# Optimization experiments

Measured on AMD Instinct MI355X. Metric: run time of the kernel, lower is better.

Reference implementation:

```python
import jax, jax.numpy as jnp
import numpy as np

NL, D, H, DFF = 6, 1024, 16, 4096
HD = D // H


def _rope(x):
    # x: [B, L, H, HD]; rotate-half RoPE applied along seq dim 1
    L = x.shape[1]
    half = HD // 2
    inv = 1.0 / (10000.0 ** (jnp.arange(half, dtype=jnp.float32) / half))
    ang = jnp.arange(L, dtype=jnp.float32)[:, None] * inv  # [L, half]
    cos = jnp.cos(ang)[None, :, None, :]
    sin = jnp.sin(ang)[None, :, None, :]
    x1, x2 = x[..., :half], x[..., half:]
    return jnp.concatenate([x1 * cos - x2 * sin, x1 * sin + x2 * cos], axis=-1)


def _ln(x, eps=1e-5):
    m = jnp.mean(x, axis=-1, keepdims=True)
    v = jnp.var(x, axis=-1, keepdims=True)
    return (x - m) * jax.lax.rsqrt(v + eps)


def _adaln(x, emb, w, b):
    # emb: [B,1,D] -> squeeze; proj -> gamma,beta
    gb = emb[:, 0, :] @ w.T + b  # [B, 2D]
    g, be = jnp.split(gb, 2, axis=-1)
    return _ln(x) * (1.0 + g[:, None, :]) + be[:, None, :]


def _attn(q, k, v, mask):
    # q:[B,Lq,H,HD] k,v:[B,Lkv,H,HD] mask:[B,Lkv] True=ignore
    scores = jnp.einsum('bqhd,bkhd->bhqk', q, k) / np.float32(np.sqrt(HD))
    scores = jnp.where(mask[:, None, None, :], jnp.float32(-jnp.inf), scores)
    w = jax.nn.softmax(scores, axis=-1)
    return jnp.einsum('bhqk,bkhd->bqhd', w, v)


def setup_inputs() -> dict:
    key = jax.random.key(0)
    ks = jax.random.split(key, 20)
    B, L, LC = 4, 1024, 512
    s = 0.02
    inp = {
        'x': jax.random.normal(ks[0], (B, L, D), jnp.float32),
        'noise_emb': jax.random.normal(ks[1], (B, 1, D), jnp.float32),
        'context': jax.random.normal(ks[2], (B, LC, D), jnp.float32),
        'src_mask': jnp.zeros((B, L), bool),
        'ctx_mask': jnp.zeros((B, LC), bool),
        'n1_w': jax.random.normal(ks[3], (NL, 2 * D, D), jnp.float32) * s,
        'n1_b': jnp.zeros((NL, 2 * D), jnp.float32),
        'n2_w': jax.random.normal(ks[4], (NL, 2 * D, D), jnp.float32) * s,
        'n2_b': jnp.zeros((NL, 2 * D), jnp.float32),
        'n3_w': jax.random.normal(ks[5], (NL, 2 * D, D), jnp.float32) * s,
        'n3_b': jnp.zeros((NL, 2 * D), jnp.float32),
        'qkv_w': jax.random.normal(ks[6], (NL, 3 * D, D), jnp.float32) * s,
        'so_w': jax.random.normal(ks[7], (NL, D, D), jnp.float32) * s,
        'cq_w': jax.random.normal(ks[8], (NL, D, D), jnp.float32) * s,
        'ck_w': jax.random.normal(ks[9], (NL, D, D), jnp.float32) * s,
        'cv_w': jax.random.normal(ks[10], (NL, D, D), jnp.float32) * s,
        'co_w': jax.random.normal(ks[11], (NL, D, D), jnp.float32) * s,
        'f1_w': jax.random.normal(ks[12], (NL, DFF, D), jnp.float32) * s,
        'f1_b': jnp.zeros((NL, DFF), jnp.float32),
        'f2_w': jax.random.normal(ks[13], (NL, D, DFF), jnp.float32) * s,
        'f2_b': jnp.zeros((NL, D), jnp.float32),
    }
    return inp


def reference(x, noise_emb, context, src_mask, ctx_mask,
              n1_w, n1_b, n2_w, n2_b, n3_w, n3_b,
              qkv_w, so_w, cq_w, ck_w, cv_w, co_w,
              f1_w, f1_b, f2_w, f2_b):
    B, L, _ = x.shape
    LC = context.shape[1]
    for i in range(NL):
        # self-attention with AdaLN pre-norm
        xn = _adaln(x, noise_emb, n1_w[i], n1_b[i])
        qkv = xn @ qkv_w[i].T  # [B,L,3D]
        q, k, v = jnp.split(qkv, 3, axis=-1)
        q = _rope(q.reshape(B, L, H, HD))
        k = _rope(k.reshape(B, L, H, HD))
        v = v.reshape(B, L, H, HD)
        a = _attn(q, k, v, src_mask).reshape(B, L, D) @ so_w[i].T
        x = x + a
        # cross-attention with AdaLN pre-norm
        xn = _adaln(x, noise_emb, n2_w[i], n2_b[i])
        q = _rope((xn @ cq_w[i].T).reshape(B, L, H, HD))
        k = _rope((context @ ck_w[i].T).reshape(B, LC, H, HD))
        v = (context @ cv_w[i].T).reshape(B, LC, H, HD)
        a = _attn(q, k, v, ctx_mask).reshape(B, L, D) @ co_w[i].T
        x = x + a
        # FFN with AdaLN pre-norm
        xn = _adaln(x, noise_emb, n3_w[i], n3_b[i])
        h = jax.nn.gelu(xn @ f1_w[i].T + f1_b[i], approximate=False)
        x = x + (h @ f2_w[i].T + f2_b[i])
    return x
```

## Files before the change

### kernel.cpp

```cpp
#include <hip/hip_runtime.h>
#include <hip/hip_bf16.h>
#include <math.h>

#define D_    1024
#define H_    16
#define HD_   64
#define NL_   6
#define DFF_  4096
#define B_    4
#define L_    1024
#define LC_   512

typedef short bf16x8 __attribute__((ext_vector_type(8)));
typedef float f32x4  __attribute__((ext_vector_type(4)));
typedef unsigned int uint32;

__device__ __forceinline__ float waveReduceSum(float v) {
#pragma unroll
  for (int off = 32; off > 0; off >>= 1) v += __shfl_xor(v, off);
  return v;
}
__device__ __forceinline__ ushort f2bf(float f) {
  union { __hip_bfloat16 h; ushort u; } c;
  c.h = __float2bfloat16(f);
  return c.u;
}
__device__ __forceinline__ float bf2f(ushort u) {
  union { uint32 i; float f; } c;
  c.i = ((uint32)u) << 16;
  return c.f;
}
__device__ __forceinline__ uint32 pk2(float a, float b) {
  return (uint32)f2bf(a) | ((uint32)f2bf(b) << 16);
}
__device__ __forceinline__ void gload16(const ushort* g, ushort* l) {
  __builtin_amdgcn_global_load_lds(
      (const __attribute__((address_space(1))) uint32*)g,
      (__attribute__((address_space(3))) uint32*)l, 16, 0, 0);
}

__global__ __launch_bounds__(256) void cvt_bf16_kernel(
    const float* __restrict__ in, ushort* __restrict__ out, int n4) {
  int i = blockIdx.x * 256 + threadIdx.x;
  int stride = gridDim.x * 256;
  for (; i < n4; i += stride) {
    float4 v = ((const float4*)in)[i];
    ushort4 o = {f2bf(v.x), f2bf(v.y), f2bf(v.z), f2bf(v.w)};
    ((ushort4*)out)[i] = o;
  }
}

__global__ __launch_bounds__(256) void cvt_pack_kv_kernel(
    const float* __restrict__ ck, const float* __restrict__ cv,
    ushort* __restrict__ out, int n4) {
  int i = blockIdx.x * 256 + threadIdx.x;
  int stride = gridDim.x * 256;
  for (; i < n4; i += stride) {
    int row = i >> 8;
    int cb = i & 255;
    int layer = row >> 11;
    int sel = (row >> 10) & 1;
    int r = row & 1023;
    const float* src = (sel ? cv : ck) +
                       (((size_t)layer << 10) + r) * 1024 + cb * 4;
    float4 v = *(const float4*)src;
    ushort4 o = {f2bf(v.x), f2bf(v.y), f2bf(v.z), f2bf(v.w)};
    ((ushort4*)out)[i] = o;
  }
}

__global__ void rope_table_kernel(float* __restrict__ tab) {
  int t = blockIdx.x * 256 + threadIdx.x;
  if (t >= L_ * 32) return;
  int l = t >> 5, j = t & 31;
  float inv = powf(10000.f, -(float)j * (1.f / 32.f));
  float ang = (float)l * inv;
  tab[l * 64 + j] = cosf(ang);
  tab[l * 64 + 32 + j] = sinf(ang);
}

__global__ __launch_bounds__(256) void adaln_gb_all_kernel(
    const float* __restrict__ emb,
    const float* __restrict__ n1w, const float* __restrict__ n2w,
    const float* __restrict__ n3w,
    const float* __restrict__ n1b, const float* __restrict__ n2b,
    const float* __restrict__ n3b,
    float* __restrict__ gb) {
  int wid = blockIdx.x * 4 + (threadIdx.x >> 6);
  int lane = threadIdx.x & 63;
  int n = wid & 2047;
  int g = wid >> 11;
  int layer = g / 3, j = g - layer * 3;
  const float* wbase = (j == 0 ? n1w : (j == 1 ? n2w : n3w));
  const float* bbase = (j == 0 ? n1b : (j == 1 ? n2b : n3b));
  const float* wr = wbase + ((size_t)layer * 2048 + n) * 1024;
  float s0 = 0.f, s1 = 0.f, s2 = 0.f, s3 = 0.f;
#pragma unroll
  for (int k4 = 0; k4 < 4; ++k4) {
    int idx = k4 * 64 + lane;
    float4 w4 = ((const float4*)wr)[idx];
    float4 e0 = ((const float4*)emb)[idx];
    float4 e1 = ((const float4*)(emb + 1024))[idx];
    float4 e2 = ((const float4*)(emb + 2048))[idx];
    float4 e3 = ((const float4*)(emb + 3072))[idx];
    s0 += w4.x * e0.x + w4.y * e0.y + w4.z * e0.z + w4.w * e0.w;
    s1 += w4.x * e1.x + w4.y * e1.y + w4.z * e1.z + w4.w * e1.w;
    s2 += w4.x * e2.x + w4.y * e2.y + w4.z * e2.z + w4.w * e2.w;
    s3 += w4.x * e3.x + w4.y * e3.y + w4.z * e3.z + w4.w * e3.w;
  }
  s0 = waveReduceSum(s0);
  s1 = waveReduceSum(s1);
  s2 = waveReduceSum(s2);
  s3 = waveReduceSum(s3);
  if (lane == 0) {
    float bb = bbase[(size_t)layer * 2048 + n];
    gb[((size_t)g * 4 + 0) * 2048 + n] = s0 + bb;
    gb[((size_t)g * 4 + 1) * 2048 + n] = s1 + bb;
    gb[((size_t)g * 4 + 2) * 2048 + n] = s2 + bb;
    gb[((size_t)g * 4 + 3) * 2048 + n] = s3 + bb;
  }
}

__global__ __launch_bounds__(256) void adaln_apply_kernel(
    const float* __restrict__ x, const float* __restrict__ gb,
    ushort* __restrict__ xn) {
  int r = blockIdx.x;
  int b = r >> 10;
  const float* xr = x + (size_t)r * D_;
  int tid = threadIdx.x;
  float4 v = *(const float4*)(xr + tid * 4);
  float s = v.x + v.y + v.z + v.w;
  float q = v.x * v.x + v.y * v.y + v.z * v.z + v.w * v.w;
  s = waveReduceSum(s);
  q = waveReduceSum(q);
  __shared__ float ssum[4], ssq[4], stats[2];
  int w = tid >> 6, lane = tid & 63;
  if (lane == 0) { ssum[w] = s; ssq[w] = q; }
  __syncthreads();
  if (tid == 0) {
    float S = ssum[0] + ssum[1] + ssum[2] + ssum[3];
    float Q = ssq[0] + ssq[1] + ssq[2] + ssq[3];
    float mean = S * (1.f / D_);
    float var = Q * (1.f / D_) - mean * mean;
    stats[0] = mean;
    stats[1] = rsqrtf(var + 1e-5f);
  }
  __syncthreads();
  float mean = stats[0], rstd = stats[1];
  const float* gp = gb + (size_t)b * 2048;
  float4 g  = *(const float4*)(gp + tid * 4);
  float4 be = *(const float4*)(gp + D_ + tid * 4);
  ushort4 o;
  o.x = f2bf((v.x - mean) * rstd * (1.f + g.x) + be.x);
  o.y = f2bf((v.y - mean) * rstd * (1.f + g.y) + be.y);
  o.z = f2bf((v.z - mean) * rstd * (1.f + g.z) + be.z);
  o.w = f2bf((v.w - mean) * rstd * (1.f + g.w) + be.w);
  *(ushort4*)(xn + (size_t)r * D_ + tid * 4) = o;
}

template <int FLAGS, bool OUTBF, int ROPE>
__global__ __launch_bounds__(256) void gemm_mfma_kernel(
    const ushort* __restrict__ A, int lda,
    const ushort* __restrict__ W, int ldw,
    const float* __restrict__ bias,
    const float* __restrict__ res, int ldres,
    void* __restrict__ Cout, int ldc, int K,
    const float* __restrict__ tab, int rlim, int lmask) {
  __shared__ __align__(16) ushort lds[24576];
  const int tid = threadIdx.x;
  const int lane = tid & 63, wv = tid >> 6;
  const int wrow = (wv >> 1) * 64, wcol = (wv & 1) * 64;
  const int fr = lane & 15;
  const int kbs = (((lane >> 4) ^ (fr & 3)) & 3) * 8;

  const int nwg = gridDim.x * gridDim.y;
  const int wg = blockIdx.y * gridDim.x + blockIdx.x;
  const int q = nwg >> 3;
  const int swz = (wg & 7) * q + (wg >> 3);
  const int row0 = (swz / gridDim.x) * 128;
  const int col0 = (swz % gridDim.x) * 128;

  const int c0 = wv * 2, c1 = wv * 2 + 1;
  const int sr = lane >> 2;
  const int sc = (((lane & 3) ^ (sr & 3)) & 3) * 8;
  const ushort* Ap0 = A + (size_t)(row0 + c0 * 16 + sr) * lda + sc;
  const ushort* Ap1 = A + (size_t)(row0 + c1 * 16 + sr) * lda + sc;
  const ushort* Wp0 = W + (size_t)(col0 + c0 * 16 + sr) * ldw + sc;
  const ushort* Wp1 = W + (size_t)(col0 + c1 * 16 + sr) * ldw + sc;

  f32x4 acc[4][4];
#pragma unroll
  for (int m = 0; m < 4; ++m)
#pragma unroll
    for (int n = 0; n < 4; ++n) acc[m][n] = (f32x4)0.f;

#define ASB(B) (lds + (B) * 4096)
#define WSB(B) (lds + 12288 + (B) * 4096)
#define STAGE(B, T)                                   \
  do {                                                \
    const int koff_ = (T) * 32;                       \
    gload16(Ap0 + koff_, ASB(B) + c0 * 512);          \
    gload16(Ap1 + koff_, ASB(B) + c1 * 512);          \
    gload16(Wp0 + koff_, WSB(B) + c0 * 512);          \
    gload16(Wp1 + koff_, WSB(B) + c1 * 512);          \
  } while (0)
#define WAITV8() asm volatile("s_waitcnt vmcnt(8)" ::: "memory")
#define WAITV4() asm volatile("s_waitcnt vmcnt(4)" ::: "memory")
#define WAITV0() asm volatile("s_waitcnt vmcnt(0)" ::: "memory")
#define BAR()    __builtin_amdgcn_s_barrier()
#define COMPUTE(B)                                                          \
  do {                                                                      \
    bf16x8 af[4], bfr[4];                                                   \
    _Pragma("unroll")                                                       \
    for (int m = 0; m < 4; ++m)                                             \
      af[m] = *(const bf16x8*)(ASB(B) + (wrow + m * 16 + fr) * 32 + kbs);   \
    _Pragma("unroll")                                                       \
    for (int n = 0; n < 4; ++n)                                             \
      bfr[n] = *(const bf16x8*)(WSB(B) + (wcol + n * 16 + fr) * 32 + kbs);  \
    _Pragma("unroll")                                                       \
    for (int m = 0; m < 4; ++m)                                             \
      _Pragma("unroll")                                                     \
      for (int n = 0; n < 4; ++n)                                           \
        acc[m][n] = __builtin_amdgcn_mfma_f32_16x16x32_bf16(af[m], bfr[n],  \
                                                            acc[m][n], 0, 0, 0); \
  } while (0)

  const int NT = K >> 5;
  STAGE(0, 0);
  STAGE(1, 1);
  for (int t = 0; t < NT; t += 3) {
    {
      const bool sA = (t + 2) < NT;
      if (sA) STAGE(2, t + 2);
      if ((t + 1) < NT) { if (sA) WAITV8(); else WAITV4(); } else WAITV0();
      BAR(); COMPUTE(0); BAR();
    }
    if ((t + 1) < NT) {
      const bool sB = (t + 3) < NT;
      if (sB) STAGE(0, t + 3);
      if ((t + 2) < NT) { if (sB) WAITV8(); else WAITV4(); } else WAITV0();
      BAR(); COMPUTE(1); BAR();
    }
    if ((t + 2) < NT) {
      const bool sC = (t + 4) < NT;
      if (sC) STAGE(1, t + 4);
      if ((t + 3) < NT) { if (sC) WAITV8(); else WAITV4(); } else WAITV0();
      BAR(); COMPUTE(2); BAR();
    }
  }
#undef STAGE
#undef WAITV8
#undef WAITV4
#undef WAITV0
#undef COMPUTE

  float bn[4];
  if (FLAGS & 1) {
#pragma unroll
    for (int n = 0; n < 4; ++n) bn[n] = bias[col0 + wcol + n * 16 + fr];
  }
#define EPI(v, n)                                                     \
  do {                                                                \
    if (FLAGS & 1) (v) += bn[n];                                      \
    if (FLAGS & 2) (v) = 0.5f * (v) * (1.f + erff((v) * 0.70710678118f)); \
  } while (0)

  if (OUTBF) {
    ushort* Ct = lds;
    ushort* Cg = (ushort*)Cout;
#pragma unroll
    for (int m = 0; m < 4; ++m) {
      int lr0 = wrow + m * 16 + (lane >> 4) * 4;
#pragma unroll
      for (int n = 0; n < 4; ++n) {
        int lc = wcol + n * 16 + fr;
#pragma unroll
        for (int r = 0; r < 4; ++r) {
          float v = acc[m][n][r];
          EPI(v, n);
          Ct[(lr0 + r) * 136 + lc] = f2bf(v);
        }
      }
    }
    __syncthreads();
#pragma unroll
    for (int it = 0; it < 8; ++it) {
      int lr = (tid >> 4) + it * 16;
      int lc = (tid & 15) * 8;
      union { int4 v; ushort us[8]; } vv;
      vv.v = *(const int4*)&Ct[lr * 136 + lc];
      if (ROPE && (col0 + lc) < rlim) {
        union { int4 v; ushort us[8]; } pv;
        pv.v = *(const int4*)&Ct[lr * 136 + (lc ^ 32)];
        int l = (row0 + lr) & lmask;
        int j = lc & 31;
        const float* cb = &tab[l * 64 + j];
        bool lowhalf = (lc & 63) < 32;
#pragma unroll
        for (int e = 0; e < 8; ++e) {
          float cc = cb[e], ss = cb[32 + e];
          float xv = bf2f(vv.us[e]), xp = bf2f(pv.us[e]);
          float o = lowhalf ? (xv * cc - xp * ss) : (xp * ss + xv * cc);
          vv.us[e] = f2bf(o);
        }
      }
      *(int4*)&Cg[(size_t)(row0 + lr) * ldc + col0 + lc] = vv.v;
    }
  } else {
    float* Cf = (float*)lds;
    float* Cg = (float*)Cout;
#pragma unroll
    for (int half = 0; half < 2; ++half) {
      if ((wv >> 1) == half) {
#pragma unroll
        for (int m = 0; m < 4; ++m) {
          int lr0 = m * 16 + (lane >> 4) * 4;
#pragma unroll
          for (int n = 0; n < 4; ++n) {
            int lc = wcol + n * 16 + fr;
#pragma unroll
            for (int r = 0; r < 4; ++r) {
              float v = acc[m][n][r];
              EPI(v, n);
              Cf[(lr0 + r) * 132 + lc] = v;
            }
          }
        }
      }
      __syncthreads();
#pragma unroll
      for (int it = 0; it < 8; ++it) {
        int lr = (tid >> 5) + it * 8;
        int lc = (tid & 31) * 4;
        int grow = row0 + half * 64 + lr;
        float4 v = *(const float4*)&Cf[lr * 132 + lc];
        if (FLAGS & 4) {
          float4 rv = *(const float4*)&res[(size_t)grow * ldres + col0 + lc];
          v.x += rv.x; v.y += rv.y; v.z += rv.z; v.w += rv.w;
        }
        *(float4*)&Cg[(size_t)grow * ldc + col0 + lc] = v;
      }
      __syncthreads();
    }
  }
#undef EPI
#undef ASB
#undef WSB
#undef BAR
}

template <int FLAGS, int ROPE>
__global__ __launch_bounds__(512, 2) void gemm256_kernel(
    const ushort* __restrict__ A, int lda,
    const ushort* __restrict__ W, int ldw,
    const float* __restrict__ bias,
    ushort* __restrict__ Cout, int ldc, int K,
    const float* __restrict__ tab, int rlim, int lmask) {
  __shared__ __align__(16) ushort lds[65536];
  const int tid = threadIdx.x;
  const int lane = tid & 63, wid = tid >> 6;
  const int wm = wid >> 2, wn = wid & 3;
  const int fr = lane & 15, hi = lane >> 4;

  const int nwg = gridDim.x * gridDim.y;
  const int wg = blockIdx.y * gridDim.x + blockIdx.x;
  const int q = nwg >> 3;
  const int swz = (wg & 7) * q + (wg >> 3);
  const int row0 = (swz / gridDim.x) * 256;
  const int col0 = (swz % gridDim.x) * 256;

  const int srow = lane >> 3;
  const int scol = ((lane & 7) ^ srow) * 8;
  const ushort* Asrc[4];
  const ushort* Wsrc[4];
#pragma unroll
  for (int j = 0; j < 4; ++j) {
    int r = wid * 32 + j * 8 + srow;
    Asrc[j] = A + (size_t)(row0 + r) * lda + scol;
    Wsrc[j] = W + (size_t)(col0 + r) * ldw + scol;
  }
#define AB256(b) (lds + (b) * 16384)
#define WB256(b) (lds + 32768 + (b) * 16384)
#define STG256(b, T)                                      \
  do {                                                    \
    const int kk_ = (T) * 64;                             \
    _Pragma("unroll")                                     \
    for (int j = 0; j < 4; ++j) {                         \
      int ch_ = wid * 4 + j;                              \
      gload16(Asrc[j] + kk_, AB256(b) + ch_ * 512);       \
      gload16(Wsrc[j] + kk_, WB256(b) + ch_ * 512);       \
    }                                                     \
  } while (0)

  f32x4 acc[8][4];
#pragma unroll
  for (int m = 0; m < 8; ++m)
#pragma unroll
    for (int n = 0; n < 4; ++n) acc[m][n] = (f32x4)0.f;

  const int NT = K >> 6;
  STG256(0, 0);
  asm volatile("s_waitcnt vmcnt(0)" ::: "memory");
  __builtin_amdgcn_s_barrier();
  for (int t = 0; t < NT; ++t) {
    const int cur = t & 1;
    if (t + 1 < NT) STG256(cur ^ 1, t + 1);
    const ushort* ab = AB256(cur);
    const ushort* wb = WB256(cur);
    __builtin_amdgcn_s_setprio(1);
#pragma unroll
    for (int s = 0; s < 2; ++s) {
      bf16x8 wf[4];
#pragma unroll
      for (int n = 0; n < 4; ++n) {
        int row = wn * 64 + n * 16 + fr;
        wf[n] = *(const bf16x8*)(wb + row * 64 + (((s * 4 + hi) ^ (fr & 7)) * 8));
      }
#pragma unroll
      for (int m = 0; m < 8; ++m) {
        int row = wm * 128 + m * 16 + fr;
        bf16x8 af = *(const bf16x8*)(ab + row * 64 + (((s * 4 + hi) ^ (fr & 7)) * 8));
#pragma unroll
        for (int n = 0; n < 4; ++n)
          acc[m][n] = __builtin_amdgcn_mfma_f32_16x16x32_bf16(af, wf[n],
                                                              acc[m][n], 0, 0, 0);
      }
    }
    __builtin_amdgcn_s_setprio(0);
    asm volatile("s_waitcnt vmcnt(0)" ::: "memory");
    __builtin_amdgcn_s_barrier();
  }
#undef STG256

  float bn[4];
  if (FLAGS & 1) {
#pragma unroll
    for (int n = 0; n < 4; ++n) bn[n] = bias[col0 + wn * 64 + n * 16 + fr];
  }
  ushort* Ct = lds;
#pragma unroll
  for (int m = 0; m < 8; ++m) {
    int lr0 = wm * 128 + m * 16 + hi * 4;
#pragma unroll
    for (int n = 0; n < 4; ++n) {
      int lc = wn * 64 + n * 16 + fr;
#pragma unroll
      for (int r = 0; r < 4; ++r) {
        float v = acc[m][n][r];
        if (FLAGS & 1) v += bn[n];
        if (FLAGS & 2) v = 0.5f * v * (1.f + erff(v * 0.70710678118f));
        Ct[(lr0 + r) * 256 + lc] = f2bf(v);
      }
    }
  }
  __syncthreads();
#pragma unroll
  for (int it = 0; it < 16; ++it) {
    int idx = tid + it * 512;
    int lr = idx >> 5;
    int lc = (idx & 31) * 8;
    union { int4 v; ushort us[8]; } vv;
    vv.v = *(const int4*)&Ct[lr * 256 + lc];
    if (ROPE && (col0 + lc) < rlim) {
      union { int4 v; ushort us[8]; } pv;
      pv.v = *(const int4*)&Ct[lr * 256 + (lc ^ 32)];
      int l = (row0 + lr) & lmask;
      int j = lc & 31;
      const float* cb = &tab[l * 64 + j];
      bool lowhalf = (lc & 63) < 32;
#pragma unroll
      for (int e = 0; e < 8; ++e) {
        float cc = cb[e], ss = cb[32 + e];
        float xv = bf2f(vv.us[e]), xp = bf2f(pv.us[e]);
        float o = lowhalf ? (xv * cc - xp * ss) : (xp * ss + xv * cc);
        vv.us[e] = f2bf(o);
      }
    }
    *(int4*)&Cout[(size_t)(row0 + lr) * ldc + col0 + lc] = vv.v;
  }
#undef AB256
#undef WB256
}

#define SWZ(row, col) (((row) << 6) + ((col) ^ (((row) & 7) << 3)))
__global__ __launch_bounds__(256) void attn_mfma_kernel(
    const ushort* __restrict__ Q, int ldq,
    const ushort* __restrict__ K, int ldk,
    const ushort* __restrict__ V, int ldv,
    ushort* __restrict__ O, int ldo,
    int Lq, int Lk, float scale) {
  __shared__ __align__(16) ushort Ks[2][64 * 64];
  __shared__ __align__(16) ushort Vt[2][64 * 64];
  __shared__ __align__(16) ushort Os[64 * 64];
  const int tid = threadIdx.x;
  const int lane = tid & 63, w = tid >> 6;
  const int fr = lane & 15, hi = lane >> 4, kb = hi * 8;
  const int b = blockIdx.z, h = blockIdx.y, q0 = blockIdx.x * 64;

  bf16x8 aq[2];
  {
    const ushort* qp = Q + (size_t)(b * Lq + q0 + w * 16 + fr) * ldq + h * 64 + kb;
    union { bf16x8 v; ushort us[8]; } t0, t1;
    t0.v = *(const bf16x8*)qp;
    t1.v = *(const bf16x8*)(qp + 32);
#pragma unroll
    for (int e = 0; e < 8; ++e) {
      t0.us[e] = f2bf(bf2f(t0.us[e]) * scale);
      t1.us[e] = f2bf(bf2f(t1.us[e]) * scale);
    }
    aq[0] = t0.v;
    aq[1] = t1.v;
  }

  const ushort* kbase = K + (size_t)(b * Lk + lane) * ldk + h * 64 + w * 16;
  const ushort* vbase = V + (size_t)(b * Lk + lane) * ldv + h * 64 + w * 16;
  int4 kr0, kr1, vr0, vr1;
#define LOADKV(T)                                          \
  do {                                                     \
    const ushort* kp_ = kbase + (size_t)(T) * 64 * ldk;    \
    kr0 = ((const int4*)kp_)[0];                           \
    kr1 = ((const int4*)kp_)[1];                           \
    const ushort* vp_ = vbase + (size_t)(T) * 64 * ldv;    \
    vr0 = ((const int4*)vp_)[0];                           \
    vr1 = ((const int4*)vp_)[1];                           \
  } while (0)
#define WRITEKV(P)                                                   \
  do {                                                               \
    *(int4*)&Ks[P][SWZ(lane, w * 16)]     = kr0;                     \
    *(int4*)&Ks[P][SWZ(lane, w * 16 + 8)] = kr1;                     \
    union { int4 v; ushort us[8]; } u0_, u1_;                        \
    u0_.v = vr0; u1_.v = vr1;                                        \
    _Pragma("unroll")                                                \
    for (int e = 0; e < 8; ++e) Vt[P][SWZ(w * 16 + e, lane)] = u0_.us[e]; \
    _Pragma("unroll")                                                \
    for (int e = 0; e < 8; ++e) Vt[P][SWZ(w * 16 + 8 + e, lane)] = u1_.us[e]; \
  } while (0)

  f32x4 oacc[4];
#pragma unroll
  for (int n = 0; n < 4; ++n) oacc[n] = (f32x4)0.f;
  float mq = -1e30f, lq = 0.f;
  const int ntiles = Lk >> 6;
  const bool lowhalf = (lane < 32);
  const bool sendSelf = (hi == 1 || hi == 2);

  LOADKV(0);
  WRITEKV(0);
  int p = 0;
  for (int t = 0; t < ntiles; ++t) {
    if (t + 1 < ntiles) LOADKV(t + 1);
    __syncthreads();

    f32x4 sacc[4];
#pragma unroll
    for (int n = 0; n < 4; ++n) sacc[n] = (f32x4)0.f;
    __builtin_amdgcn_s_setprio(1);
#pragma unroll
    for (int s = 0; s < 2; ++s) {
#pragma unroll
      for (int n = 0; n < 4; ++n) {
        bf16x8 ak = *(const bf16x8*)&Ks[p][SWZ(n * 16 + fr, s * 32 + kb)];
        sacc[n] = __builtin_amdgcn_mfma_f32_16x16x32_bf16(ak, aq[s], sacc[n], 0, 0, 0);
      }
    }
    __builtin_amdgcn_s_setprio(0);

    float sm = sacc[0][0];
#pragma unroll
    for (int n = 0; n < 4; ++n)
#pragma unroll
      for (int r = 0; r < 4; ++r) sm = fmaxf(sm, sacc[n][r]);
    sm = fmaxf(sm, __shfl_xor(sm, 16));
    sm = fmaxf(sm, __shfl_xor(sm, 32));
    float mnew = fmaxf(mq, sm);
    float corrq = __expf(mq - mnew);
    mq = mnew;
    float pe[4][4];
    float psum = 0.f;
#pragma unroll
    for (int n = 0; n < 4; ++n)
#pragma unroll
      for (int r = 0; r < 4; ++r) {
        pe[n][r] = __expf(sacc[n][r] - mnew);
        psum += pe[n][r];
      }
    psum += __shfl_xor(psum, 16);
    psum += __shfl_xor(psum, 32);
    lq = lq * corrq + psum;
    float c0 = __shfl(corrq, hi * 4 + 0);
    float c1 = __shfl(corrq, hi * 4 + 1);
    float c2 = __shfl(corrq, hi * 4 + 2);
    float c3 = __shfl(corrq, hi * 4 + 3);
#pragma unroll
    for (int n = 0; n < 4; ++n) {
      oacc[n][0] *= c0; oacc[n][1] *= c1; oacc[n][2] *= c2; oacc[n][3] *= c3;
    }

    uint32 u00 = pk2(pe[0][0], pe[0][1]), u01 = pk2(pe[0][2], pe[0][3]);
    uint32 u10 = pk2(pe[1][0], pe[1][1]), u11 = pk2(pe[1][2], pe[1][3]);
    uint32 u20 = pk2(pe[2][0], pe[2][1]), u21 = pk2(pe[2][2], pe[2][3]);
    uint32 u30 = pk2(pe[3][0], pe[3][1]), u31 = pk2(pe[3][2], pe[3][3]);
    uint32 selfw0 = lowhalf ? u00 : u10;
    uint32 selfw1 = lowhalf ? u01 : u11;
    uint32 selfw2 = lowhalf ? u20 : u30;
    uint32 selfw3 = lowhalf ? u21 : u31;
    uint32 send10 = lowhalf ? u10 : u00;
    uint32 send11 = lowhalf ? u11 : u01;
    uint32 send12 = lowhalf ? u30 : u20;
    uint32 send13 = lowhalf ? u31 : u21;
    uint32 farw0 = __shfl_xor((int)send10, 32);
    uint32 farw1 = __shfl_xor((int)send11, 32);
    uint32 farw2 = __shfl_xor((int)send12, 32);
    uint32 farw3 = __shfl_xor((int)send13, 32);
    uint32 s20 = sendSelf ? selfw0 : farw0;
    uint32 s21 = sendSelf ? selfw1 : farw1;
    uint32 s22 = sendSelf ? selfw2 : farw2;
    uint32 s23 = sendSelf ? selfw3 : farw3;
    uint32 rcv0 = __shfl_xor((int)s20, 16);
    uint32 rcv1 = __shfl_xor((int)s21, 16);
    uint32 rcv2 = __shfl_xor((int)s22, 16);
    uint32 rcv3 = __shfl_xor((int)s23, 16);
    union { uint32 wd[4]; bf16x8 v; } pa0, pa1;
    if (hi == 0) {
      pa0.wd[0] = selfw0; pa0.wd[1] = selfw1; pa0.wd[2] = rcv0; pa0.wd[3] = rcv1;
      pa1.wd[0] = selfw2; pa1.wd[1] = selfw3; pa1.wd[2] = rcv2; pa1.wd[3] = rcv3;
    } else if (hi == 1) {
      pa0.wd[0] = rcv0; pa0.wd[1] = rcv1; pa0.wd[2] = farw0; pa0.wd[3] = farw1;
      pa1.wd[0] = rcv2; pa1.wd[1] = rcv3; pa1.wd[2] = farw2; pa1.wd[3] = farw3;
    } else if (hi == 2) {
      pa0.wd[0] = farw0; pa0.wd[1] = farw1; pa0.wd[2] = rcv0; pa0.wd[3] = rcv1;
      pa1.wd[0] = farw2; pa1.wd[1] = farw3; pa1.wd[2] = rcv2; pa1.wd[3] = rcv3;
    } else {
      pa0.wd[0] = rcv0; pa0.wd[1] = rcv1; pa0.wd[2] = selfw0; pa0.wd[3] = selfw1;
      pa1.wd[0] = rcv2; pa1.wd[1] = rcv3; pa1.wd[2] = selfw2; pa1.wd[3] = selfw3;
    }

    __builtin_amdgcn_s_setprio(1);
#pragma unroll
    for (int n = 0; n < 4; ++n) {
      bf16x8 bv0 = *(const bf16x8*)&Vt[p][SWZ(n * 16 + fr, 0 * 32 + kb)];
      oacc[n] = __builtin_amdgcn_mfma_f32_16x16x32_bf16(pa0.v, bv0, oacc[n], 0, 0, 0);
      bf16x8 bv1 = *(const bf16x8*)&Vt[p][SWZ(n * 16 + fr, 1 * 32 + kb)];
      oacc[n] = __builtin_amdgcn_mfma_f32_16x16x32_bf16(pa1.v, bv1, oacc[n], 0, 0, 0);
    }
    __builtin_amdgcn_s_setprio(0);

    __syncthreads();
    if (t + 1 < ntiles) WRITEKV(p ^ 1);
    p ^= 1;
  }
#undef LOADKV
#undef WRITEKV

  float linv[4];
#pragma unroll
  for (int r = 0; r < 4; ++r) linv[r] = 1.f / __shfl(lq, hi * 4 + r);
#pragma unroll
  for (int r = 0; r < 4; ++r) {
    int rl = w * 16 + hi * 4 + r;
#pragma unroll
    for (int n = 0; n < 4; ++n)
      Os[SWZ(rl, n * 16 + fr)] = f2bf(oacc[n][r] * linv[r]);
  }
  __syncthreads();
  {
    int row = tid >> 2, cbk = (tid & 3) * 16;
    ushort* op = O + (size_t)(b * Lq + q0 + row) * ldo + h * 64 + cbk;
    int4 o0 = *(const int4*)&Os[SWZ(row, cbk)];
    int4 o1 = *(const int4*)&Os[SWZ(row, cbk + 8)];
    ((int4*)op)[0] = o0;
    ((int4*)op)[1] = o1;
  }
}

extern "C" void kernel_launch(void* const* d_in, const int* in_sizes, int n_in,
                              void* d_out, int out_size, void* d_ws, size_t ws_size,
                              hipStream_t stream) {
  const float* x_in = (const float*)d_in[0];
  const float* emb  = (const float*)d_in[1];
  const float* ctx  = (const float*)d_in[2];
  const float* n1w = (const float*)d_in[5];
  const float* n1b = (const float*)d_in[6];
  const float* n2w = (const float*)d_in[7];
  const float* n2b = (const float*)d_in[8];
  const float* n3w = (const float*)d_in[9];
  const float* n3b = (const float*)d_in[10];
  const float* qkvw = (const float*)d_in[11];
  const float* sow  = (const float*)d_in[12];
  const float* cqw  = (const float*)d_in[13];
  const float* ckw  = (const float*)d_in[14];
  const float* cvw  = (const float*)d_in[15];
  const float* cow  = (const float*)d_in[16];
  const float* f1w  = (const float*)d_in[17];
  const float* f1b  = (const float*)d_in[18];
  const float* f2w  = (const float*)d_in[19];
  const float* f2b  = (const float*)d_in[20];

  float* xcur = (float*)d_out;

  ushort* xnb  = (ushort*)d_ws;
  ushort* big  = xnb + (size_t)4096 * 1024;
  ushort* obb  = big + (size_t)4096 * 4096;
  ushort* kvb  = obb + (size_t)4096 * 1024;
  ushort* ctxb = kvb + (size_t)2048 * 2048;
  float*  gball= (float*)(ctxb + (size_t)2048 * 1024);
  float*  tab  = gball + 18 * 4 * 2048;
  ushort* scrW = (ushort*)(tab + 65536);
  const size_t SZ_QKV = (size_t)NL_ * 3072 * 1024;
  const size_t SZ_SQ  = (size_t)NL_ * 1024 * 1024;
  const size_t SZ_F   = (size_t)NL_ * 4096 * 1024;
  ushort* wqkv = scrW + (size_t)4096 * 1024;
  ushort* wso  = wqkv + SZ_QKV;
  ushort* wcq  = wso + SZ_SQ;
  ushort* wkv  = wcq + SZ_SQ;
  ushort* wco  = wkv + 2 * SZ_SQ;
  ushort* wf1  = wco + SZ_SQ;
  ushort* wf2  = wf1 + SZ_F;
  const size_t need_full = (size_t)((char*)(wf2 + SZ_F) - (char*)d_ws);
  const bool wbfull = (ws_size >= need_full);

  hipMemcpyAsync(xcur, x_in, (size_t)B_ * L_ * D_ * sizeof(float),
                 hipMemcpyDeviceToDevice, stream);
  rope_table_kernel<<<128, 256, 0, stream>>>(tab);
  adaln_gb_all_kernel<<<9216, 256, 0, stream>>>(emb, n1w, n2w, n3w,
                                                n1b, n2b, n3b, gball);
  cvt_bf16_kernel<<<1024, 256, 0, stream>>>(ctx, ctxb,
                                            (int)((size_t)2048 * 1024 / 4));

  if (wbfull) {
    cvt_bf16_kernel<<<2048, 256, 0, stream>>>(qkvw, wqkv, (int)(SZ_QKV / 4));
    cvt_bf16_kernel<<<2048, 256, 0, stream>>>(sow,  wso,  (int)(SZ_SQ / 4));
    cvt_bf16_kernel<<<2048, 256, 0, stream>>>(cqw,  wcq,  (int)(SZ_SQ / 4));
    cvt_pack_kv_kernel<<<2048, 256, 0, stream>>>(ckw, cvw, wkv,
                                                 (int)(2 * SZ_SQ / 4));
    cvt_bf16_kernel<<<2048, 256, 0, stream>>>(cow,  wco,  (int)(SZ_SQ / 4));
    cvt_bf16_kernel<<<2048, 256, 0, stream>>>(f1w,  wf1,  (int)(SZ_F / 4));
    cvt_bf16_kernel<<<2048, 256, 0, stream>>>(f2w,  wf2,  (int)(SZ_F / 4));
  }

  auto prepW = [&](const float* src, ushort* full, size_t layerOff,
                   size_t nelem) -> const ushort* {
    if (wbfull) return full + layerOff;
    cvt_bf16_kernel<<<1024, 256, 0, stream>>>(src + layerOff, scrW,
                                              (int)(nelem / 4));
    return scrW;
  };

  const int ROWS = B_ * L_;
  const dim3 blk(256);
  const dim3 blk512(512);

  for (int i = 0; i < NL_; ++i) {
    const float* f1bi = f1b + (size_t)i * DFF_;
    const float* f2bi = f2b + (size_t)i * D_;

    adaln_apply_kernel<<<ROWS, blk, 0, stream>>>(
        xcur, gball + (size_t)(i * 3 + 0) * 4 * 2048, xnb);
    gemm256_kernel<0, 1><<<dim3(12, 16), blk512, 0, stream>>>(
        xnb, D_, prepW(qkvw, wqkv, (size_t)i * 3072 * 1024, (size_t)3072 * 1024),
        D_, nullptr, big, 3072, D_, tab, 2048, 1023);
    attn_mfma_kernel<<<dim3(L_ / 64, H_, B_), blk, 0, stream>>>(
        big, 3072, big + 1024, 3072, big + 2048, 3072, obb, D_, L_, L_, 0.125f);
    gemm_mfma_kernel<4, false, 0><<<dim3(8, 32), blk, 0, stream>>>(
        obb, D_, prepW(sow, wso, (size_t)i * 1024 * 1024, (size_t)1024 * 1024),
        D_, nullptr, xcur, D_, xcur, D_, D_, tab, 0, 0);

    adaln_apply_kernel<<<ROWS, blk, 0, stream>>>(
        xcur, gball + (size_t)(i * 3 + 1) * 4 * 2048, xnb);
    gemm_mfma_kernel<0, true, 1><<<dim3(8, 32), blk, 0, stream>>>(
        xnb, D_, prepW(cqw, wcq, (size_t)i * 1024 * 1024, (size_t)1024 * 1024),
        D_, nullptr, nullptr, 0, big, 1024, D_, tab, 1024, 1023);
    {
      const ushort* wkvi;
      if (wbfull) {
        wkvi = wkv + (size_t)i * 2048 * 1024;
      } else {
        cvt_bf16_kernel<<<512, 256, 0, stream>>>(
            ckw + (size_t)i * 1024 * 1024, scrW, (int)((size_t)1024 * 1024 / 4));
        cvt_bf16_kernel<<<512, 256, 0, stream>>>(
            cvw + (size_t)i * 1024 * 1024, scrW + (size_t)1024 * 1024,
            (int)((size_t)1024 * 1024 / 4));
        wkvi = scrW;
      }
      gemm_mfma_kernel<0, true, 1><<<dim3(16, 16), blk, 0, stream>>>(
          ctxb, D_, wkvi, D_, nullptr, nullptr, 0, kvb, 2048, D_, tab, 1024, 511);
    }
    attn_mfma_kernel<<<dim3(L_ / 64, H_, B_), blk, 0, stream>>>(
        big, 1024, kvb, 2048, kvb + 1024, 2048, obb, D_, L_, LC_, 0.125f);
    gemm_mfma_kernel<4, false, 0><<<dim3(8, 32), blk, 0, stream>>>(
        obb, D_, prepW(cow, wco, (size_t)i * 1024 * 1024, (size_t)1024 * 1024),
        D_, nullptr, xcur, D_, xcur, D_, D_, tab, 0, 0);

    adaln_apply_kernel<<<ROWS, blk, 0, stream>>>(
        xcur, gball + (size_t)(i * 3 + 2) * 4 * 2048, xnb);
    gemm256_kernel<3, 0><<<dim3(16, 16), blk512, 0, stream>>>(
        xnb, D_, prepW(f1w, wf1, (size_t)i * 4096 * 1024, (size_t)4096 * 1024),
        D_, f1bi, big, DFF_, D_, tab, 0, 0);
    gemm_mfma_kernel<5, false, 0><<<dim3(8, 32), blk, 0, stream>>>(
        big, DFF_, prepW(f2w, wf2, (size_t)i * 4096 * 1024, (size_t)4096 * 1024),
        DFF_, f2bi, xcur, D_, xcur, D_, DFF_, tab, 0, 0);
  }
}
```

Baseline: 2.164 ms.

## Use 128-query attention blocks with split K/V loaders and banded XCD GEMM tile order

The attention kernel now runs 512 threads covering 128 query rows per block. Four waves load K and the other four load and transpose V, so each K/V tile fetched into LDS serves twice as many queries and the per-thread load and transpose work is halved. Separately, both GEMM kernels remap workgroups after the XCD swizzle into bands four tile-rows tall, so neighbouring workgroups share A and W tiles in L2. The cost is a doubled output staging buffer in LDS and half as many attention blocks, which may reduce occupancy and parallelism.

```diff
diff --git a/kernel.cpp b/kernel.cpp
--- a/kernel.cpp
+++ b/kernel.cpp
@@ -37,6 +37,18 @@
   __builtin_amdgcn_global_load_lds(
       (const __attribute__((address_space(1))) uint32*)g,
       (__attribute__((address_space(3))) uint32*)l, 16, 0, 0);
+}
+
+__device__ __forceinline__ void xcd_banded(int& trow, int& tcol) {
+  const int nwg = gridDim.x * gridDim.y;
+  const int wg = blockIdx.y * gridDim.x + blockIdx.x;
+  const int q = nwg >> 3;
+  const int swz = (wg & 7) * q + (wg >> 3);
+  const int bandw = gridDim.x * 4;
+  const int band = swz / bandw;
+  const int rem = swz % bandw;
+  trow = band * 4 + (rem & 3);
+  tcol = rem >> 2;
 }
 
 __global__ __launch_bounds__(256) void cvt_bf16_kernel(
@@ -173,12 +185,10 @@
   const int fr = lane & 15;
   const int kbs = (((lane >> 4) ^ (fr & 3)) & 3) * 8;
 
-  const int nwg = gridDim.x * gridDim.y;
-  const int wg = blockIdx.y * gridDim.x + blockIdx.x;
-  const int q = nwg >> 3;
-  const int swz = (wg & 7) * q + (wg >> 3);
-  const int row0 = (swz / gridDim.x) * 128;
-  const int col0 = (swz % gridDim.x) * 128;
+  int trow, tcol;
+  xcd_banded(trow, tcol);
+  const int row0 = trow * 128;
+  const int col0 = tcol * 128;
 
   const int c0 = wv * 2, c1 = wv * 2 + 1;
   const int sr = lane >> 2;
@@ -362,12 +372,10 @@
   const int wm = wid >> 2, wn = wid & 3;
   const int fr = lane & 15, hi = lane >> 4;
 
-  const int nwg = gridDim.x * gridDim.y;
-  const int wg = blockIdx.y * gridDim.x + blockIdx.x;
-  const int q = nwg >> 3;
-  const int swz = (wg & 7) * q + (wg >> 3);
-  const int row0 = (swz / gridDim.x) * 256;
-  const int col0 = (swz % gridDim.x) * 256;
+  int trow, tcol;
+  xcd_banded(trow, tcol);
+  const int row0 = trow * 256;
+  const int col0 = tcol * 256;
 
   const int srow = lane >> 3;
   const int scol = ((lane & 7) ^ srow) * 8;
@@ -483,7 +491,7 @@
 }
 
 #define SWZ(row, col) (((row) << 6) + ((col) ^ (((row) & 7) << 3)))
-__global__ __launch_bounds__(256) void attn_mfma_kernel(
+__global__ __launch_bounds__(512) void attn_mfma_kernel(
     const ushort* __restrict__ Q, int ldq,
     const ushort* __restrict__ K, int ldk,
     const ushort* __restrict__ V, int ldv,
@@ -491,11 +499,13 @@
     int Lq, int Lk, float scale) {
   __shared__ __align__(16) ushort Ks[2][64 * 64];
   __shared__ __align__(16) ushort Vt[2][64 * 64];
-  __shared__ __align__(16) ushort Os[64 * 64];
+  __shared__ __align__(16) ushort Os[128 * 64];
   const int tid = threadIdx.x;
   const int lane = tid & 63, w = tid >> 6;
   const int fr = lane & 15, hi = lane >> 4, kb = hi * 8;
-  const int b = blockIdx.z, h = blockIdx.y, q0 = blockIdx.x * 64;
+  const int b = blockIdx.z, h = blockIdx.y, q0 = blockIdx.x * 128;
+  const int kw = w & 3;
+  const bool isK = (w < 4);
 
   bf16x8 aq[2];
   {
@@ -512,28 +522,30 @@
     aq[1] = t1.v;
   }
 
-  const ushort* kbase = K + (size_t)(b * Lk + lane) * ldk + h * 64 + w * 16;
-  const ushort* vbase = V + (size_t)(b * Lk + lane) * ldv + h * 64 + w * 16;
-  int4 kr0, kr1, vr0, vr1;
-#define LOADKV(T)                                          \
-  do {                                                     \
-    const ushort* kp_ = kbase + (size_t)(T) * 64 * ldk;    \
-    kr0 = ((const int4*)kp_)[0];                           \
-    kr1 = ((const int4*)kp_)[1];                           \
-    const ushort* vp_ = vbase + (size_t)(T) * 64 * ldv;    \
-    vr0 = ((const int4*)vp_)[0];                           \
-    vr1 = ((const int4*)vp_)[1];                           \
+  const int ldkv = isK ? ldk : ldv;
+  const ushort* kvbase = (isK ? K : V) + (size_t)(b * Lk + lane) * ldkv
+                         + h * 64 + kw * 16;
+  const size_t kvstep = (size_t)64 * ldkv;
+  int4 r0, r1;
+#define LOADKV(T)                                      \
+  do {                                                 \
+    const ushort* p_ = kvbase + (size_t)(T) * kvstep;  \
+    r0 = ((const int4*)p_)[0];                         \
+    r1 = ((const int4*)p_)[1];                         \
   } while (0)
-#define WRITEKV(P)                                                   \
-  do {                                                               \
-    *(int4*)&Ks[P][SWZ(lane, w * 16)]     = kr0;                     \
-    *(int4*)&Ks[P][SWZ(lane, w * 16 + 8)] = kr1;                     \
-    union { int4 v; ushort us[8]; } u0_, u1_;                        \
-    u0_.v = vr0; u1_.v = vr1;                                        \
-    _Pragma("unroll")                                                \
-    for (int e = 0; e < 8; ++e) Vt[P][SWZ(w * 16 + e, lane)] = u0_.us[e]; \
-    _Pragma("unroll")                                                \
-    for (int e = 0; e < 8; ++e) Vt[P][SWZ(w * 16 + 8 + e, lane)] = u1_.us[e]; \
+#define WRITEKV(P)                                                        \
+  do {                                                                    \
+    if (isK) {                                                            \
+      *(int4*)&Ks[P][SWZ(lane, kw * 16)]     = r0;                        \
+      *(int4*)&Ks[P][SWZ(lane, kw * 16 + 8)] = r1;                        \
+    } else {                                                              \
+      union { int4 v; ushort us[8]; } u0_, u1_;                           \
+      u0_.v = r0; u1_.v = r1;                                             \
+      _Pragma("unroll")                                                   \
+      for (int e = 0; e < 8; ++e) Vt[P][SWZ(kw * 16 + e, lane)] = u0_.us[e]; \
+      _Pragma("unroll")                                                   \
+      for (int e = 0; e < 8; ++e) Vt[P][SWZ(kw * 16 + 8 + e, lane)] = u1_.us[e]; \
+    }                                                                     \
   } while (0)
 
   f32x4 oacc[4];
@@ -759,7 +771,7 @@
     gemm256_kernel<0, 1><<<dim3(12, 16), blk512, 0, stream>>>(
         xnb, D_, prepW(qkvw, wqkv, (size_t)i * 3072 * 1024, (size_t)3072 * 1024),
         D_, nullptr, big, 3072, D_, tab, 2048, 1023);
-    attn_mfma_kernel<<<dim3(L_ / 64, H_, B_), blk, 0, stream>>>(
+    attn_mfma_kernel<<<dim3(L_ / 128, H_, B_), blk512, 0, stream>>>(
         big, 3072, big + 1024, 3072, big + 2048, 3072, obb, D_, L_, L_, 0.125f);
     gemm_mfma_kernel<4, false, 0><<<dim3(8, 32), blk, 0, stream>>>(
         obb, D_, prepW(sow, wso, (size_t)i * 1024 * 1024, (size_t)1024 * 1024),
@@ -785,7 +797,7 @@
       gemm_mfma_kernel<0, true, 1><<<dim3(16, 16), blk, 0, stream>>>(
           ctxb, D_, wkvi, D_, nullptr, nullptr, 0, kvb, 2048, D_, tab, 1024, 511);
     }
-    attn_mfma_kernel<<<dim3(L_ / 64, H_, B_), blk, 0, stream>>>(
+    attn_mfma_kernel<<<dim3(L_ / 128, H_, B_), blk512, 0, stream>>>(
         big, 1024, kvb, 2048, kvb + 1024, 2048, obb, D_, L_, LC_, 0.125f);
     gemm_mfma_kernel<4, false, 0><<<dim3(8, 32), blk, 0, stream>>>(
         obb, D_, prepW(cow, wco, (size_t)i * 1024 * 1024, (size_t)1024 * 1024),
```

Result: faster. 2.053 ms (-5.1%).
